# Kernel tuning notes

Hardware: AMD Instinct MI355X
Metric: run time of the kernel (lower is better)

The kernel has to match this reference:

```python
import math
import jax, jax.numpy as jnp
import numpy as np

NP_, NA_ = 100000, 50000
IN_DIM = OUT_DIM = 128
H, DK = 4, 32
E_CITES, E_WRITES, E_REV = 600000, 300000, 300000


def setup_inputs() -> dict:
    key = jax.random.key(0)
    ks = jax.random.split(key, 16)
    s_in = 1.0 / math.sqrt(IN_DIM)   # ~ Linear default init scale
    s_dk = 1.0 / math.sqrt(DK)       # ~ xavier for d_k x d_k
    return {
        "h_paper": jax.random.normal(ks[0], (NP_, IN_DIM), jnp.float32),
        "h_author": jax.random.normal(ks[1], (NA_, IN_DIM), jnp.float32),
        "Wk": jax.random.normal(ks[2], (2, OUT_DIM, IN_DIM), jnp.float32) * s_in,
        "bk": jnp.zeros((2, OUT_DIM), jnp.float32),
        "Wq": jax.random.normal(ks[3], (2, OUT_DIM, IN_DIM), jnp.float32) * s_in,
        "bq": jnp.zeros((2, OUT_DIM), jnp.float32),
        "Wv": jax.random.normal(ks[4], (2, OUT_DIM, IN_DIM), jnp.float32) * s_in,
        "bv": jnp.zeros((2, OUT_DIM), jnp.float32),
        "Wa": jax.random.normal(ks[5], (2, OUT_DIM, OUT_DIM), jnp.float32) * s_in,
        "ba": jnp.zeros((2, OUT_DIM), jnp.float32),
        "rel_att": jax.random.normal(ks[6], (3, H, DK, DK), jnp.float32) * s_dk,
        "rel_msg": jax.random.normal(ks[7], (3, H, DK, DK), jnp.float32) * s_dk,
        "rel_pri": jnp.ones((3, H), jnp.float32),
        "skip": jnp.ones((2,), jnp.float32),
        "cites_src": jax.random.randint(ks[8], (E_CITES,), 0, NP_, jnp.int32),
        "cites_dst": jax.random.randint(ks[9], (E_CITES,), 0, NP_, jnp.int32),
        "writes_src": jax.random.randint(ks[10], (E_WRITES,), 0, NA_, jnp.int32),
        "writes_dst": jax.random.randint(ks[11], (E_WRITES,), 0, NP_, jnp.int32),
        "rev_src": jax.random.randint(ks[12], (E_REV,), 0, NP_, jnp.int32),
        "rev_dst": jax.random.randint(ks[13], (E_REV,), 0, NA_, jnp.int32),
    }


def _seg_softmax(scores, seg, n):
    # edge softmax normalized by destination node (DGL edge_softmax, norm_by='dst')
    m = jax.ops.segment_max(scores, seg, num_segments=n)
    e = jnp.exp(scores - m[seg])
    z = jax.ops.segment_sum(e, seg, num_segments=n)
    return e / z[seg]


def reference(h_paper, h_author, Wk, bk, Wq, bq, Wv, bv, Wa, ba,
              rel_att, rel_msg, rel_pri, skip,
              cites_src, cites_dst, writes_src, writes_dst, rev_src, rev_dst):
    sqrt_dk = math.sqrt(DK)

    def proj(h, W, b, t):
        return (h @ W[t].T + b[t]).reshape(-1, H, DK)  # [N, H, dk]

    def rel_agg(h_src, h_dst, ts, td, e, src, dst, n_dst):
        # relation-specific transforms of k and v (per-head dk x dk matmul)
        k = jnp.einsum('nhi,hij->nhj', proj(h_src, Wk, bk, ts), rel_att[e])
        v = jnp.einsum('nhi,hij->nhj', proj(h_src, Wv, bv, ts), rel_msg[e])
        q = proj(h_dst, Wq, bq, td)
        # per-edge attention logits: (q_dst . k_src) * pri / sqrt(dk)  -> [E, H]
        score = jnp.einsum('ehd,ehd->eh', q[dst], k[src]) * rel_pri[e] / sqrt_dk
        a = _seg_softmax(score, dst, n_dst)
        # weighted scatter-sum of messages to destination nodes
        return jax.ops.segment_sum(v[src] * a[:, :, None], dst, num_segments=n_dst)

    # cross_reducer='mean': average per-relation aggregates per dst node type
    t_paper = (rel_agg(h_paper, h_paper, 0, 0, 0, cites_src, cites_dst, NP_) +
               rel_agg(h_author, h_paper, 1, 0, 1, writes_src, writes_dst, NP_)) * 0.5
    t_author = rel_agg(h_paper, h_author, 0, 1, 2, rev_src, rev_dst, NA_)

    def out(t, h, nt):
        trans = t.reshape(-1, OUT_DIM) @ Wa[nt].T + ba[nt]  # dropout = identity (eval)
        alpha = jax.nn.sigmoid(skip[nt])
        return trans * alpha + h * (1.0 - alpha)

    return jnp.concatenate([out(t_paper, h_paper, 0), out(t_author, h_author, 1)], axis=0)
```

## Files before the change

kernel.cpp:

```cpp
#include <hip/hip_runtime.h>
#include <hip/hip_bf16.h>
#include <math.h>

#define NP 100000
#define NA 50000
#define DIM 128
#define NH 4
#define DKK 32
#define EC 600000
#define EW 300000
#define ER 300000
#define CAP 32
#define SCL 0.17677669529663687f

#define CDIV(a,b) (((a)+(b)-1)/(b))

typedef __attribute__((ext_vector_type(8))) short bf16x8;
typedef __attribute__((ext_vector_type(4))) float f32x4;
typedef __attribute__((ext_vector_type(2))) float f32x2;

__device__ __forceinline__ ushort f2b(float f){
  unsigned u = __float_as_uint(f);
  unsigned r = u + 0x7FFFu + ((u>>16)&1u);
  return (ushort)(r>>16);
}
__device__ __forceinline__ float blo(unsigned u){ return __uint_as_float(u<<16); }
__device__ __forceinline__ float bhi(unsigned u){ return __uint_as_float(u & 0xFFFF0000u); }

struct C2Args { const float4* in[2]; uint2* out[2]; };
__global__ void k_cast2(C2Args a){
  int s = blockIdx.y;
  int i = blockIdx.x*256 + threadIdx.x;
  float4 v = a.in[s][i];
  uint2 o;
  o.x = (unsigned)f2b(v.x) | ((unsigned)f2b(v.y)<<16);
  o.y = (unsigned)f2b(v.z) | ((unsigned)f2b(v.w)<<16);
  a.out[s][i] = o;
}

__global__ void k_zero_i(int* p, int n){
  int i = blockIdx.x*blockDim.x + threadIdx.x;
  if (i < n) p[i] = 0;
}

__global__ void k_fuse(const float* __restrict__ Wk, const float* __restrict__ bk,
                       const float* __restrict__ Wv, const float* __restrict__ bv,
                       const float* __restrict__ rel_att, const float* __restrict__ rel_msg,
                       ushort* __restrict__ Wfb_all, float* __restrict__ bfu_all){
  int rel = blockIdx.x >> 7;
  int ts = (rel==1) ? 1 : 0;
  ushort* Wfb = Wfb_all + rel*32768;
  float*  bfu = bfu_all + rel*256;
  int idx = (blockIdx.x & 127)*256 + threadIdx.x;
  int which = idx >> 14;
  int rem = idx & 16383;
  int op = rem >> 7;
  int j  = rem & 127;
  int h = op >> 5, jp = op & 31;
  const float* W  = which ? Wv : Wk;
  const float* R  = which ? rel_msg : rel_att;
  const float* Wt = W + (size_t)ts*DIM*DIM;
  const float* Re = R + (((size_t)rel*NH + h)*DKK)*DKK + jp;
  float acc = 0.f;
  #pragma unroll
  for (int i=0;i<DKK;i++) acc += Wt[(h*DKK+i)*DIM + j] * Re[(size_t)i*DKK];
  Wfb[which*16384 + op*DIM + j] = f2b(acc);
  if (idx < 256){
    int w2 = idx >> 7; int op2 = idx & 127; int h2 = op2>>5, jp2 = op2&31;
    const float* bsrc = (w2 ? bv : bk) + (size_t)ts*DIM;
    const float* R2 = (w2 ? rel_msg : rel_att) + (((size_t)rel*NH + h2)*DKK)*DKK + jp2;
    float accb = 0.f;
    #pragma unroll
    for (int i=0;i<DKK;i++) accb += bsrc[h2*DKK+i]*R2[(size_t)i*DKK];
    bfu[w2*DIM + op2] = accb;
  }
}

struct MArgs {
  const float* X[3];
  const ushort* W[3][3];
  const float* b[3][3];
  ushort* Y[3][3];
  int N[3];
  int npan[3];
  int base[3];
};
__global__ __launch_bounds__(512) void k_mega(MArgs g){
  int b = blockIdx.x;
  int seg = (b >= g.base[2]) ? 2 : ((b >= g.base[1]) ? 1 : 0);
  int local = b - g.base[seg];
  int N = g.N[seg];
  int tile = local*64;
  if (tile >= N) return;
  int tid = threadIdx.x;
  int wv = tid >> 6, l = tid & 63;
  int lr = l & 15, lk = l >> 4;
  int rowg = wv >> 1, colg = wv & 1;
  int arow = tile + rowg*16 + lr;
  int ar = (arow < N) ? arow : 0;
  const float4* Ar = (const float4*)(g.X[seg] + (size_t)ar*DIM);
  bf16x8 A[4];
  #pragma unroll
  for (int kc=0;kc<4;kc++){
    float4 u = Ar[kc*8 + lk*2];
    float4 v = Ar[kc*8 + lk*2 + 1];
    bf16x8 a;
    a[0]=(short)f2b(u.x); a[1]=(short)f2b(u.y); a[2]=(short)f2b(u.z); a[3]=(short)f2b(u.w);
    a[4]=(short)f2b(v.x); a[5]=(short)f2b(v.y); a[6]=(short)f2b(v.z); a[7]=(short)f2b(v.w);
    A[kc] = a;
  }
  __shared__ __align__(16) ushort Wl[128*136];
  __shared__ __align__(16) ushort Ost[64*136];
  uint4* Wl4 = (uint4*)Wl;
  int npan = g.npan[seg];
  for (int p=0; p<npan; ++p){
    const uint4* Ws = (const uint4*)g.W[seg][p];
    #pragma unroll
    for (int i=0;i<4;i++){
      int idx = i*512 + tid;
      uint4 v = Ws[idx];
      int r = idx >> 4, c = idx & 15;
      Wl4[r*17 + c] = v;
    }
    __syncthreads();
    const float* bias = g.b[seg][p];
    #pragma unroll
    for (int ct=0; ct<4; ct++){
      int col = colg*64 + ct*16 + lr;
      f32x4 acc = {0.f,0.f,0.f,0.f};
      #pragma unroll
      for (int kc=0;kc<4;kc++){
        bf16x8 B = *(const bf16x8*)&Wl[col*136 + kc*32 + lk*8];
        acc = __builtin_amdgcn_mfma_f32_16x16x32_bf16(A[kc], B, acc, 0, 0, 0);
      }
      float bv = bias[col];
      #pragma unroll
      for (int j=0;j<4;j++)
        Ost[(rowg*16 + lk*4 + j)*136 + col] = f2b(acc[j] + bv);
    }
    __syncthreads();
    int orow = tid >> 3;
    int oseg = (tid & 7)*2;
    int grow = tile + orow;
    if (grow < N){
      uint4* dst = (uint4*)(g.Y[seg][p] + (size_t)grow*DIM);
      const uint4* s = (const uint4*)Ost;
      dst[oseg]   = s[orow*17 + oseg];
      dst[oseg+1] = s[orow*17 + oseg + 1];
    }
    __syncthreads();
  }
}

struct BArgs { const int* dst[3]; const int* src[3]; int* cnt[3]; int* slots[3]; int E[3]; int n[3]; };
__global__ void k_bucket(BArgs a){
  int r = blockIdx.y;
  int E = a.E[r], n = a.n[r];
  const int* dst = a.dst[r];
  const int* srcv = a.src[r];
  int* cnt = a.cnt[r];
  int* slots = a.slots[r];
  int g = blockIdx.x & 7;
  int sub = blockIdx.x >> 3;
  int chunk = (n + 7) >> 3;
  int lo = g*chunk;
  int hi = lo + chunk; if (hi > n) hi = n;
  int per = (E + 255) >> 8;
  per = (per + 3) & ~3;
  int e0 = sub*per;
  int e1 = e0 + per; if (e1 > E) e1 = E;
  for (int i = e0 + threadIdx.x*4; i < e1; i += 256*4){
    if (i + 4 <= e1){
      int4 d = *(const int4*)(dst + i);
      int4 s = *(const int4*)(srcv + i);
      if (d.x>=lo && d.x<hi){ int p=atomicAdd(&cnt[d.x],1); if(p<CAP) slots[(size_t)d.x*CAP+p]=s.x; }
      if (d.y>=lo && d.y<hi){ int p=atomicAdd(&cnt[d.y],1); if(p<CAP) slots[(size_t)d.y*CAP+p]=s.y; }
      if (d.z>=lo && d.z<hi){ int p=atomicAdd(&cnt[d.z],1); if(p<CAP) slots[(size_t)d.z*CAP+p]=s.z; }
      if (d.w>=lo && d.w<hi){ int p=atomicAdd(&cnt[d.w],1); if(p<CAP) slots[(size_t)d.w*CAP+p]=s.w; }
    } else {
      for (int j=i; j<e1; ++j){
        int d = dst[j];
        if (d>=lo && d<hi){ int p=atomicAdd(&cnt[d],1); if(p<CAP) slots[(size_t)d*CAP+p]=srcv[j]; }
      }
    }
  }
}

__device__ __forceinline__ void agg_bucket(const unsigned* __restrict__ K2,
    const unsigned* __restrict__ V2, const int* __restrict__ slots,
    int deg, int nsrc, float qx, float qy, int lane,
    f32x2& av, float& z)
{
  const int4* sl4 = (const int4*)slots;
  for (int i = 0; i < deg; i += 4){
    int4 s4 = sl4[i>>2];
    int s0 = ((unsigned)s4.x < (unsigned)nsrc) ? s4.x : 0;
    int s1 = ((unsigned)s4.y < (unsigned)nsrc) ? s4.y : 0;
    int s2 = ((unsigned)s4.z < (unsigned)nsrc) ? s4.z : 0;
    int s3 = ((unsigned)s4.w < (unsigned)nsrc) ? s4.w : 0;
    bool v1 = (i+1 < deg), v2 = (i+2 < deg), v3 = (i+3 < deg);
    unsigned ku0 = K2[(size_t)s0*64 + lane];
    unsigned ku1 = K2[(size_t)s1*64 + lane];
    unsigned ku2 = K2[(size_t)s2*64 + lane];
    unsigned ku3 = K2[(size_t)s3*64 + lane];
    unsigned vu0 = V2[(size_t)s0*64 + lane];
    unsigned vu1 = V2[(size_t)s1*64 + lane];
    unsigned vu2 = V2[(size_t)s2*64 + lane];
    unsigned vu3 = V2[(size_t)s3*64 + lane];
    float p0 = qx*blo(ku0) + qy*bhi(ku0);
    float p1 = qx*blo(ku1) + qy*bhi(ku1);
    float p2 = qx*blo(ku2) + qy*bhi(ku2);
    float p3 = qx*blo(ku3) + qy*bhi(ku3);
    #pragma unroll
    for (int d=1; d<16; d<<=1){
      p0 += __shfl_xor(p0, d);
      p1 += __shfl_xor(p1, d);
      p2 += __shfl_xor(p2, d);
      p3 += __shfl_xor(p3, d);
    }
    float e0 = __expf(p0);
    float e1 = v1 ? __expf(p1) : 0.f;
    float e2 = v2 ? __expf(p2) : 0.f;
    float e3 = v3 ? __expf(p3) : 0.f;
    z += (e0+e1)+(e2+e3);
    f32x2 w0 = {blo(vu0), bhi(vu0)};
    f32x2 w1 = {blo(vu1), bhi(vu1)};
    f32x2 w2 = {blo(vu2), bhi(vu2)};
    f32x2 w3 = {blo(vu3), bhi(vu3)};
    av += (w0*e0 + w1*e1) + (w2*e2 + w3*e3);
  }
}

__global__ __launch_bounds__(256) void k_attnM2(
    const unsigned* __restrict__ QP, const unsigned* __restrict__ QA,
    const unsigned* __restrict__ K0, const unsigned* __restrict__ V0,
    const unsigned* __restrict__ K1, const unsigned* __restrict__ V1,
    const unsigned* __restrict__ K2, const unsigned* __restrict__ V2,
    const int* __restrict__ slots_all, const int* __restrict__ cnt_all,
    const float* __restrict__ pri, float* __restrict__ t_paper, float* __restrict__ t_author)
{
  int w = blockIdx.x*4 + (threadIdx.x>>6);
  if (w >= NP+NA) return;
  int lane = threadIdx.x & 63;
  int h = lane >> 4;
  if (w < NP){
    unsigned qu = QP[(size_t)w*64 + lane];
    float qx = blo(qu), qy = bhi(qu);
    float s0f = pri[h]*SCL, s1f = pri[NH+h]*SCL;
    int d0 = cnt_all[w];      if (d0 > CAP) d0 = CAP;
    int d1 = cnt_all[NP + w]; if (d1 > CAP) d1 = CAP;
    f32x2 x = {0.f,0.f}, y = {0.f,0.f};
    float zx = 0.f, zy = 0.f;
    agg_bucket(K0, V0, slots_all + (size_t)w*CAP,      d0, NP, qx*s0f, qy*s0f, lane, x, zx);
    agg_bucket(K1, V1, slots_all + ((size_t)NP+w)*CAP, d1, NA, qx*s1f, qy*s1f, lane, y, zy);
    float ix = (zx > 0.f) ? 1.f/zx : 0.f;
    float iy = (zy > 0.f) ? 1.f/zy : 0.f;
    f32x2 o = x*ix + y*iy;
    ((f32x2*)t_paper)[(size_t)w*64 + lane] = o;
  } else {
    int wn = w - NP;
    unsigned qu = QA[(size_t)wn*64 + lane];
    float qx = blo(qu), qy = bhi(qu);
    float s2f = pri[2*NH+h]*SCL;
    int d2 = cnt_all[2*NP + wn]; if (d2 > CAP) d2 = CAP;
    f32x2 r = {0.f,0.f};
    float zr = 0.f;
    agg_bucket(K2, V2, slots_all + ((size_t)2*NP+wn)*CAP, d2, NP, qx*s2f, qy*s2f, lane, r, zr);
    float ir = (zr > 0.f) ? 1.f/zr : 0.f;
    f32x2 o = r*ir;
    ((f32x2*)t_author)[(size_t)wn*64 + lane] = o;
  }
}

struct FArgs { const float* X[2]; const ushort* W[2]; const float* b[2]; const float* h[2];
               float* out[2]; float scale[2]; int N[2]; const float* skip; };
__global__ __launch_bounds__(256) void k_fingemm(FArgs g){
  int y = blockIdx.y;
  int N = g.N[y];
  if ((int)blockIdx.x*32 >= N) return;
  const float* X = g.X[y];
  const ushort* Wb = g.W[y];
  const float* bias = g.b[y];
  const float* hin = g.h[y];
  float* out = g.out[y];
  float scale = g.scale[y];
  int tid = threadIdx.x;
  int wv = tid >> 6;
  int l  = tid & 63;
  int lr = l & 15, lk = l >> 4;
  int r0 = blockIdx.x*32 + (wv&1)*16;
  int c0 = (wv>>1)*64;
  int arow = r0 + lr;
  int ar = (arow < N) ? arow : 0;
  const float4* Ar = (const float4*)(X + (size_t)ar*DIM);
  bf16x8 A[4];
  #pragma unroll
  for (int kc=0;kc<4;kc++){
    float4 u = Ar[kc*8 + lk*2];
    float4 v = Ar[kc*8 + lk*2 + 1];
    bf16x8 a;
    a[0]=(short)f2b(u.x); a[1]=(short)f2b(u.y); a[2]=(short)f2b(u.z); a[3]=(short)f2b(u.w);
    a[4]=(short)f2b(v.x); a[5]=(short)f2b(v.y); a[6]=(short)f2b(v.z); a[7]=(short)f2b(v.w);
    A[kc] = a;
  }
  __shared__ float Ls[32][132];
  #pragma unroll
  for (int ct=0; ct<4; ct++){
    int col = c0 + ct*16 + lr;
    const bf16x8* Wrow = (const bf16x8*)(Wb + (size_t)col*DIM);
    f32x4 acc = {0.f,0.f,0.f,0.f};
    #pragma unroll
    for (int kc=0;kc<4;kc++)
      acc = __builtin_amdgcn_mfma_f32_16x16x32_bf16(A[kc], Wrow[kc*4+lk], acc, 0, 0, 0);
    float bv = bias[col];
    #pragma unroll
    for (int j=0;j<4;j++){
      int lrow = (wv&1)*16 + lk*4 + j;
      Ls[lrow][col] = scale*acc[j] + bv;
    }
  }
  __syncthreads();
  float alpha = 1.f/(1.f + expf(-g.skip[y]));
  float beta  = 1.f - alpha;
  int orow = tid >> 3;
  int ocb  = (tid & 7)*16;
  int row  = blockIdx.x*32 + orow;
  if (row < N){
    const float4* H4 = (const float4*)hin;
    float4* O4 = (float4*)out;
    #pragma unroll
    for (int q=0;q<4;q++){
      float4 tv = *(const float4*)&Ls[orow][ocb + q*4];
      float4 hv = H4[(size_t)row*32 + (ocb>>2) + q];
      float4 o;
      o.x = alpha*tv.x + beta*hv.x;
      o.y = alpha*tv.y + beta*hv.y;
      o.z = alpha*tv.z + beta*hv.z;
      o.w = alpha*tv.w + beta*hv.w;
      O4[(size_t)row*32 + (ocb>>2) + q] = o;
    }
  }
}

extern "C" void kernel_launch(void* const* d_in, const int* in_sizes, int n_in,
                              void* d_out, int out_size, void* d_ws, size_t ws_size,
                              hipStream_t stream) {
  const float* h_paper = (const float*)d_in[0];
  const float* h_author= (const float*)d_in[1];
  const float* Wk = (const float*)d_in[2];
  const float* bk = (const float*)d_in[3];
  const float* Wq = (const float*)d_in[4];
  const float* bq = (const float*)d_in[5];
  const float* Wv = (const float*)d_in[6];
  const float* bv = (const float*)d_in[7];
  const float* Wa = (const float*)d_in[8];
  const float* ba = (const float*)d_in[9];
  const float* rel_att = (const float*)d_in[10];
  const float* rel_msg = (const float*)d_in[11];
  const float* rel_pri = (const float*)d_in[12];
  const float* skip    = (const float*)d_in[13];
  const int* cites_src = (const int*)d_in[14];
  const int* cites_dst = (const int*)d_in[15];
  const int* writes_src= (const int*)d_in[16];
  const int* writes_dst= (const int*)d_in[17];
  const int* rev_src   = (const int*)d_in[18];
  const int* rev_dst   = (const int*)d_in[19];

  ushort* qbP = (ushort*)d_ws;
  ushort* qbA = qbP + (size_t)NP*DIM;
  ushort* K0  = qbA + (size_t)NA*DIM;
  ushort* V0  = K0  + (size_t)NP*DIM;
  ushort* K1  = V0  + (size_t)NP*DIM;
  ushort* V1  = K1  + (size_t)NA*DIM;
  ushort* K2  = V1  + (size_t)NA*DIM;
  ushort* V2  = K2  + (size_t)NP*DIM;
  ushort* Wqb = V2  + (size_t)NP*DIM;
  ushort* Wab = Wqb + 32768;
  ushort* Wfb = Wab + 32768;
  float*  bfu = (float*)(Wfb + 3*32768);
  int* ib = (int*)(bfu + 3*256);
  const int NDST_TOT = 2*NP + NA;
  int* cnt_all   = ib;           ib += NDST_TOT;
  int* slots_all = ib;

  float* t_paper  = (float*)d_out;
  float* t_author = (float*)d_out + (size_t)NP*DIM;

  const int cntB[3] = {0, NP, 2*NP};

  {
    C2Args a;
    a.in[0]=(const float4*)Wq; a.out[0]=(uint2*)Wqb;
    a.in[1]=(const float4*)Wa; a.out[1]=(uint2*)Wab;
    k_cast2<<<dim3(32,2),256,0,stream>>>(a);
  }
  k_fuse<<<384,256,0,stream>>>(Wk, bk, Wv, bv, rel_att, rel_msg, Wfb, bfu);
  k_zero_i<<<CDIV(NDST_TOT,256),256,0,stream>>>(cnt_all, NDST_TOT);
  {
    BArgs b;
    const int* dsts[3] = {cites_dst, writes_dst, rev_dst};
    const int* srcs[3] = {cites_src, writes_src, rev_src};
    int Es[3] = {EC, EW, ER};
    int ns[3] = {NP, NP, NA};
    for (int r=0;r<3;r++){
      b.dst[r]=dsts[r]; b.src[r]=srcs[r];
      b.cnt[r]=cnt_all+cntB[r];
      b.slots[r]=slots_all+(size_t)cntB[r]*CAP;
      b.E[r]=Es[r]; b.n[r]=ns[r];
    }
    k_bucket<<<dim3(2048,3),256,0,stream>>>(b);
  }
  {
    const int T0 = CDIV(NP,64), T1 = CDIV(NA,64), T2 = CDIV(NP,64);
    MArgs m;
    m.base[0]=0; m.base[1]=T0; m.base[2]=T0+T1;
    m.X[0]=h_paper;  m.N[0]=NP; m.npan[0]=3;
    m.W[0][0]=Wqb;        m.b[0][0]=bq;        m.Y[0][0]=qbP;
    m.W[0][1]=Wfb;        m.b[0][1]=bfu;       m.Y[0][1]=K0;
    m.W[0][2]=Wfb+16384;  m.b[0][2]=bfu+DIM;   m.Y[0][2]=V0;
    m.X[1]=h_author; m.N[1]=NA; m.npan[1]=3;
    m.W[1][0]=Wqb+16384;        m.b[1][0]=bq+DIM;        m.Y[1][0]=qbA;
    m.W[1][1]=Wfb+32768;        m.b[1][1]=bfu+256;       m.Y[1][1]=K1;
    m.W[1][2]=Wfb+32768+16384;  m.b[1][2]=bfu+256+DIM;   m.Y[1][2]=V1;
    m.X[2]=h_paper;  m.N[2]=NP; m.npan[2]=2;
    m.W[2][0]=Wfb+2*32768;        m.b[2][0]=bfu+512;       m.Y[2][0]=K2;
    m.W[2][1]=Wfb+2*32768+16384;  m.b[2][1]=bfu+512+DIM;   m.Y[2][1]=V2;
    m.W[2][2]=Wfb;                m.b[2][2]=bfu;           m.Y[2][2]=K2;
    k_mega<<<T0+T1+T2,512,0,stream>>>(m);
  }
  k_attnM2<<<CDIV(NP+NA,4),256,0,stream>>>(
      (const unsigned*)qbP, (const unsigned*)qbA,
      (const unsigned*)K0, (const unsigned*)V0,
      (const unsigned*)K1, (const unsigned*)V1,
      (const unsigned*)K2, (const unsigned*)V2,
      slots_all, cnt_all, rel_pri, t_paper, t_author);
  {
    FArgs f;
    f.X[0]=t_paper;   f.W[0]=Wab;        f.b[0]=ba;     f.h[0]=h_paper;
    f.out[0]=t_paper;  f.scale[0]=0.5f; f.N[0]=NP;
    f.X[1]=t_author;  f.W[1]=Wab+16384;  f.b[1]=ba+DIM; f.h[1]=h_author;
    f.out[1]=t_author; f.scale[1]=1.0f; f.N[1]=NA;
    f.skip = skip;
    k_fingemm<<<dim3(CDIV(NP,32),2),256,0,stream>>>(f);
  }
}
```

Baseline: 354.7 us.

## Make projection GEMM persistent per weight panel with grid-stride row tiles

Restructures the projection GEMM so each block owns one weight panel (one of eight Q/K/V jobs), loads it and its bias into shared memory/registers once, then grid-strides over 64-row tiles. This removes repeated per-tile weight panel loads and the per-panel synchronization. In exchange, input rows are now read and converted to bf16 once per panel rather than once per tile, raising global input traffic.

```diff
diff --git a/kernel.cpp b/kernel.cpp
--- a/kernel.cpp
+++ b/kernel.cpp
@@ -76,54 +76,49 @@
   }
 }
 
-struct MArgs {
-  const float* X[3];
-  const ushort* W[3][3];
-  const float* b[3][3];
-  ushort* Y[3][3];
-  int N[3];
-  int npan[3];
-  int base[3];
-};
+struct MJob { const float* X; const ushort* W; const float* b; ushort* Y; int N; };
+struct MArgs { MJob j[8]; int bps; };
 __global__ __launch_bounds__(512) void k_mega(MArgs g){
-  int b = blockIdx.x;
-  int seg = (b >= g.base[2]) ? 2 : ((b >= g.base[1]) ? 1 : 0);
-  int local = b - g.base[seg];
-  int N = g.N[seg];
-  int tile = local*64;
-  if (tile >= N) return;
+  int stream = blockIdx.x / g.bps;
+  int t0 = blockIdx.x % g.bps;
+  MJob jb = g.j[stream];
+  int ntiles = CDIV(jb.N, 64);
   int tid = threadIdx.x;
+  __shared__ __align__(16) ushort Wl[128*136];
+  __shared__ __align__(16) ushort Ost[64*136];
+  uint4* Wl4 = (uint4*)Wl;
+  {
+    const uint4* Ws = (const uint4*)jb.W;
+    #pragma unroll
+    for (int i=0;i<4;i++){
+      int idx = i*512 + tid;
+      Wl4[(idx>>4)*17 + (idx&15)] = Ws[idx];
+    }
+  }
   int wv = tid >> 6, l = tid & 63;
   int lr = l & 15, lk = l >> 4;
   int rowg = wv >> 1, colg = wv & 1;
-  int arow = tile + rowg*16 + lr;
-  int ar = (arow < N) ? arow : 0;
-  const float4* Ar = (const float4*)(g.X[seg] + (size_t)ar*DIM);
-  bf16x8 A[4];
+  float bvr[4];
   #pragma unroll
-  for (int kc=0;kc<4;kc++){
-    float4 u = Ar[kc*8 + lk*2];
-    float4 v = Ar[kc*8 + lk*2 + 1];
-    bf16x8 a;
-    a[0]=(short)f2b(u.x); a[1]=(short)f2b(u.y); a[2]=(short)f2b(u.z); a[3]=(short)f2b(u.w);
-    a[4]=(short)f2b(v.x); a[5]=(short)f2b(v.y); a[6]=(short)f2b(v.z); a[7]=(short)f2b(v.w);
-    A[kc] = a;
-  }
-  __shared__ __align__(16) ushort Wl[128*136];
-  __shared__ __align__(16) ushort Ost[64*136];
-  uint4* Wl4 = (uint4*)Wl;
-  int npan = g.npan[seg];
-  for (int p=0; p<npan; ++p){
-    const uint4* Ws = (const uint4*)g.W[seg][p];
-    #pragma unroll
-    for (int i=0;i<4;i++){
-      int idx = i*512 + tid;
-      uint4 v = Ws[idx];
-      int r = idx >> 4, c = idx & 15;
-      Wl4[r*17 + c] = v;
-    }
-    __syncthreads();
-    const float* bias = g.b[seg][p];
+  for (int ct=0; ct<4; ct++) bvr[ct] = jb.b[colg*64 + ct*16 + lr];
+  __syncthreads();
+  int orow = tid >> 3;
+  int oseg = (tid & 7)*2;
+  for (int t = t0; t < ntiles; t += g.bps){
+    int tile = t*64;
+    int arow = tile + rowg*16 + lr;
+    int ar = (arow < jb.N) ? arow : 0;
+    const float4* Ar = (const float4*)(jb.X + (size_t)ar*DIM);
+    bf16x8 A[4];
+    #pragma unroll
+    for (int kc=0;kc<4;kc++){
+      float4 u = Ar[kc*8 + lk*2];
+      float4 v = Ar[kc*8 + lk*2 + 1];
+      bf16x8 a;
+      a[0]=(short)f2b(u.x); a[1]=(short)f2b(u.y); a[2]=(short)f2b(u.z); a[3]=(short)f2b(u.w);
+      a[4]=(short)f2b(v.x); a[5]=(short)f2b(v.y); a[6]=(short)f2b(v.z); a[7]=(short)f2b(v.w);
+      A[kc] = a;
+    }
     #pragma unroll
     for (int ct=0; ct<4; ct++){
       int col = colg*64 + ct*16 + lr;
@@ -133,17 +128,14 @@
         bf16x8 B = *(const bf16x8*)&Wl[col*136 + kc*32 + lk*8];
         acc = __builtin_amdgcn_mfma_f32_16x16x32_bf16(A[kc], B, acc, 0, 0, 0);
       }
-      float bv = bias[col];
       #pragma unroll
       for (int j=0;j<4;j++)
-        Ost[(rowg*16 + lk*4 + j)*136 + col] = f2b(acc[j] + bv);
+        Ost[(rowg*16 + lk*4 + j)*136 + col] = f2b(acc[j] + bvr[ct]);
     }
     __syncthreads();
-    int orow = tid >> 3;
-    int oseg = (tid & 7)*2;
     int grow = tile + orow;
-    if (grow < N){
-      uint4* dst = (uint4*)(g.Y[seg][p] + (size_t)grow*DIM);
+    if (grow < jb.N){
+      uint4* dst = (uint4*)(jb.Y + (size_t)grow*DIM);
       const uint4* s = (const uint4*)Ost;
       dst[oseg]   = s[orow*17 + oseg];
       dst[oseg+1] = s[orow*17 + oseg + 1];
@@ -411,22 +403,18 @@
     k_bucket<<<dim3(2048,3),256,0,stream>>>(b);
   }
   {
-    const int T0 = CDIV(NP,64), T1 = CDIV(NA,64), T2 = CDIV(NP,64);
+    const int BPS = 96;
     MArgs m;
-    m.base[0]=0; m.base[1]=T0; m.base[2]=T0+T1;
-    m.X[0]=h_paper;  m.N[0]=NP; m.npan[0]=3;
-    m.W[0][0]=Wqb;        m.b[0][0]=bq;        m.Y[0][0]=qbP;
-    m.W[0][1]=Wfb;        m.b[0][1]=bfu;       m.Y[0][1]=K0;
-    m.W[0][2]=Wfb+16384;  m.b[0][2]=bfu+DIM;   m.Y[0][2]=V0;
-    m.X[1]=h_author; m.N[1]=NA; m.npan[1]=3;
-    m.W[1][0]=Wqb+16384;        m.b[1][0]=bq+DIM;        m.Y[1][0]=qbA;
-    m.W[1][1]=Wfb+32768;        m.b[1][1]=bfu+256;       m.Y[1][1]=K1;
-    m.W[1][2]=Wfb+32768+16384;  m.b[1][2]=bfu+256+DIM;   m.Y[1][2]=V1;
-    m.X[2]=h_paper;  m.N[2]=NP; m.npan[2]=2;
-    m.W[2][0]=Wfb+2*32768;        m.b[2][0]=bfu+512;       m.Y[2][0]=K2;
-    m.W[2][1]=Wfb+2*32768+16384;  m.b[2][1]=bfu+512+DIM;   m.Y[2][1]=V2;
-    m.W[2][2]=Wfb;                m.b[2][2]=bfu;           m.Y[2][2]=K2;
-    k_mega<<<T0+T1+T2,512,0,stream>>>(m);
+    m.bps = BPS;
+    m.j[0] = { h_paper,  Wqb,                bq,          qbP, NP };
+    m.j[1] = { h_paper,  Wfb,                bfu,         K0,  NP };
+    m.j[2] = { h_paper,  Wfb+16384,          bfu+DIM,     V0,  NP };
+    m.j[3] = { h_author, Wqb+16384,          bq+DIM,      qbA, NA };
+    m.j[4] = { h_author, Wfb+32768,          bfu+256,     K1,  NA };
+    m.j[5] = { h_author, Wfb+32768+16384,    bfu+256+DIM, V1,  NA };
+    m.j[6] = { h_paper,  Wfb+2*32768,        bfu+512,     K2,  NP };
+    m.j[7] = { h_paper,  Wfb+2*32768+16384,  bfu+512+DIM, V2,  NP };
+    k_mega<<<8*BPS,512,0,stream>>>(m);
   }
   k_attnM2<<<CDIV(NP+NA,4),256,0,stream>>>(
       (const unsigned*)qbP, (const unsigned*)qbA,
```

New measurement: 381.0 us. +7.4%, slower.
